# Optimization experiments

Measured on AMD Instinct MI355X. Metric: run time of the kernel, lower is better.

Reference implementation:

```python
import jax, jax.numpy as jnp
import numpy as np

N_HEADS = 16


def build_bd3lm_mask(n, block_size, dtype):
    """BD3LM mask for concatenated [xt | x0] input of length 2n.
    0 = attend, finfo.min = masked. Shape (2n, 2n)."""
    idx = jnp.arange(2 * n)
    q_idx = idx[:, None]
    kv_idx = idx[None, :]
    x0_q = q_idx >= n
    x0_kv = kv_idx >= n
    block_q = jnp.where(x0_q, (q_idx - n) // block_size, q_idx // block_size)
    block_kv = jnp.where(x0_kv, (kv_idx - n) // block_size, kv_idx // block_size)
    block_diagonal = (block_q == block_kv) & (x0_q == x0_kv)
    offset_block_causal = (block_q > block_kv) & x0_kv & (~x0_q)
    block_causal = (block_q >= block_kv) & x0_kv & x0_q
    can_attend = block_diagonal | offset_block_causal | block_causal
    neg = jnp.finfo(dtype).min
    return jnp.where(can_attend, jnp.array(0, dtype), jnp.array(neg, dtype))


def setup_inputs() -> dict:
    key = jax.random.key(0)
    ks = jax.random.split(key, 5)
    B, T, D = 4, 2048, 1024  # T = 2*L, L = 1024
    s = 1.0 / np.sqrt(D)
    return {
        "x": jax.random.normal(ks[0], (B, T, D), jnp.float32),
        "Wq": jax.random.normal(ks[1], (D, D), jnp.float32) * s,
        "bq": jnp.zeros((D,), jnp.float32),
        "Wk": jax.random.normal(ks[2], (D, D), jnp.float32) * s,
        "bk": jnp.zeros((D,), jnp.float32),
        "Wv": jax.random.normal(ks[3], (D, D), jnp.float32) * s,
        "bv": jnp.zeros((D,), jnp.float32),
        "Wo": jax.random.normal(ks[4], (D, D), jnp.float32) * s,
        "bo": jnp.zeros((D,), jnp.float32),
        "block_size": 4,
    }


def reference(x, Wq, bq, Wk, bk, Wv, bv, Wo, bo, block_size):
    B, T, D = x.shape
    H = N_HEADS
    hd = D // H
    n = T // 2  # length of each copy in [xt | x0]
    mask = build_bd3lm_mask(n, block_size, x.dtype)  # (T, T)

    def split_heads(t):  # (B, T, D) -> (B, H, T, hd)
        return t.reshape(B, T, H, hd).transpose(0, 2, 1, 3)

    q = split_heads(x @ Wq + bq) * (hd ** -0.5)
    k = split_heads(x @ Wk + bk)
    v = split_heads(x @ Wv + bv)
    scores = jnp.einsum("bhqd,bhkd->bhqk", q, k) + mask[None, None]
    attn = jax.nn.softmax(scores, axis=-1)
    ctx = jnp.einsum("bhqk,bhkd->bhqd", attn, v)
    ctx = ctx.transpose(0, 2, 1, 3).reshape(B, T, D)
    return ctx @ Wo + bo
```

## Files before the change

kernel.cpp:

```cpp
#include <hip/hip_runtime.h>
#include <hip/hip_bf16.h>
#include <stdint.h>

typedef __hip_bfloat16 bf16;
typedef short v8s __attribute__((ext_vector_type(8)));
typedef float v4f __attribute__((ext_vector_type(4)));

#define TT   2048
#define DD   1024
#define HH   16
#define HDIM 64
#define NN   1024
#define MASKV (-1e9f)
#define QSCALE 0.18033688011112042f

#if __has_builtin(__builtin_amdgcn_exp2f)
#define EXP2F(x) __builtin_amdgcn_exp2f(x)
#else
#define EXP2F(x) exp2f(x)
#endif

__device__ __forceinline__ v4f mfma16x16x32(v8s a, v8s b, v4f c) {
    return __builtin_amdgcn_mfma_f32_16x16x32_bf16(a, b, c, 0, 0, 0);
}

template<bool SW>
__device__ __forceinline__ v4f MM(v8s a, v8s b, v4f c) {
    if constexpr (SW)
        return __builtin_amdgcn_mfma_f32_16x16x32_bf16(b, a, c, 0, 0, 0);
    else
        return __builtin_amdgcn_mfma_f32_16x16x32_bf16(a, b, c, 0, 0, 0);
}

#define GLDS16(lds, g)                                                          \
    __builtin_amdgcn_global_load_lds(                                           \
        (const __attribute__((address_space(1))) void*)(g),                     \
        (__attribute__((address_space(3))) void*)(lds), 16, 0, 0)

__device__ __forceinline__ bf16 f2b(float f) { return __float2bfloat16(f); }

__global__ __launch_bounds__(256) void prep(
    const float* __restrict__ x,  bf16* __restrict__ xb,
    const float* __restrict__ w0, const float* __restrict__ w1,
    const float* __restrict__ w2, const float* __restrict__ w3,
    bf16* __restrict__ dst)
{
    __shared__ float tile[64][65];
    const int b = blockIdx.x, tid = threadIdx.x;

    if (b < 8192) {
        const size_t i = ((size_t)b * 256 + tid) * 4;
        const float4 f = *(const float4*)(x + i);
        union { bf16 bb[4]; uint64_t u; } cv;
        cv.bb[0] = f2b(f.x); cv.bb[1] = f2b(f.y);
        cv.bb[2] = f2b(f.z); cv.bb[3] = f2b(f.w);
        *(uint64_t*)(xb + i) = cv.u;
        return;
    }

    const int b2 = b - 8192;
    const int z  = b2 >> 8;
    const int rem = b2 & 255;
    const int c0 = (rem & 15) * 64, r0 = (rem >> 4) * 64;
    const float* src = (z == 0) ? w0 : (z == 1) ? w1 : (z == 2) ? w2 : w3;
    bf16* d = dst + (size_t)z * 1024 * 1024;
    const int tx = tid & 63, ty = tid >> 6;
#pragma unroll
    for (int j = 0; j < 16; j++) {
        int r = ty + j * 4;
        tile[r][tx] = src[(size_t)(r0 + r) * 1024 + c0 + tx];
    }
    __syncthreads();
#pragma unroll
    for (int j = 0; j < 16; j++) {
        int r = ty + j * 4;
        d[(size_t)(c0 + r) * 1024 + r0 + tx] = f2b(tile[tx][r]);
    }
}

template<bool SW>
__device__ __forceinline__ void gemm_core_256x128(
    const bf16* __restrict__ A, const bf16* __restrict__ BT,
    const int m0, const int n0, const int K,
    bf16* __restrict__ As, bf16* __restrict__ Bs,
    v4f (&acc)[8][2])
{
    const int tid  = threadIdx.x;
    const int lane = tid & 63, wv = tid >> 6;
    const int quad = lane >> 4, c = lane & 15;
    const int wm = wv >> 2, wn = wv & 3;
    const int c7 = c & 7;
    const int NT = K >> 6;

    const int rloc = wv * 8 + (lane >> 3);
    const int gsw  = ((lane & 7) ^ ((lane >> 3) & 7)) << 3;
    const bf16* aSrc = A  + (size_t)(m0 + rloc) * K + gsw;
    const bf16* bSrc = BT + (size_t)(n0 + rloc) * K + gsw;

#pragma unroll
    for (int i = 0; i < 8; i++)
#pragma unroll
        for (int j = 0; j < 2; j++) acc[i][j] = (v4f){0.f, 0.f, 0.f, 0.f};

    auto stageA = [&](bf16* dst, int j, int kt) {
        const int mo = ((j & 1) << 7) | ((j >> 1) << 6);
        GLDS16(dst + (j * 64 + wv * 8) * 64, aSrc + (size_t)mo * K + kt * 64);
    };
    auto stageB = [&](bf16* dst, int j, int kt) {
        GLDS16(dst + (j * 64 + wv * 8) * 64, bSrc + (size_t)(j << 6) * K + kt * 64);
    };

    stageB(Bs, 0, 0); stageB(Bs, 1, 0);
    stageA(As, 0, 0); stageA(As, 1, 0); stageA(As, 2, 0); stageA(As, 3, 0);
    asm volatile("s_waitcnt vmcnt(2)" ::: "memory");
    asm volatile("s_barrier" ::: "memory");

#pragma unroll 1
    for (int kt = 0; kt < NT; ++kt) {
        bf16* Ac = As + (kt & 1) * 16384;
        bf16* Bc = Bs + (kt & 1) * 8192;
        bf16* An = As + ((kt & 1) ^ 1) * 16384;
        bf16* Bn = Bs + ((kt & 1) ^ 1) * 8192;
        const int ktn = (kt + 1 < NT) ? kt + 1 : kt;

        v8s bfr[2][2];
#pragma unroll
        for (int nt = 0; nt < 2; nt++)
#pragma unroll
            for (int kh = 0; kh < 2; kh++)
                bfr[nt][kh] = *(const v8s*)(Bc + (wn * 32 + nt * 16 + c) * 64
                                            + (((kh * 4 + quad) ^ c7) << 3));
        v8s af[4][2];
#pragma unroll
        for (int mt = 0; mt < 4; mt++)
#pragma unroll
            for (int kh = 0; kh < 2; kh++)
                af[mt][kh] = *(const v8s*)(Ac + (wm * 64 + mt * 16 + c) * 64
                                           + (((kh * 4 + quad) ^ c7) << 3));
        stageB(Bn, 0, ktn); stageB(Bn, 1, ktn); stageA(An, 0, ktn);
        asm volatile("s_barrier" ::: "memory");
        __builtin_amdgcn_s_setprio(1);
#pragma unroll
        for (int mt = 0; mt < 4; mt++)
#pragma unroll
            for (int nt = 0; nt < 2; nt++) {
                acc[mt][nt] = MM<SW>(af[mt][0], bfr[nt][0], acc[mt][nt]);
                acc[mt][nt] = MM<SW>(af[mt][1], bfr[nt][1], acc[mt][nt]);
            }
        __builtin_amdgcn_s_setprio(0);
        asm volatile("s_waitcnt vmcnt(3)" ::: "memory");
        asm volatile("s_barrier" ::: "memory");

#pragma unroll
        for (int mt = 0; mt < 4; mt++)
#pragma unroll
            for (int kh = 0; kh < 2; kh++)
                af[mt][kh] = *(const v8s*)(Ac + (128 + wm * 64 + mt * 16 + c) * 64
                                           + (((kh * 4 + quad) ^ c7) << 3));
        stageA(An, 1, ktn); stageA(An, 2, ktn); stageA(An, 3, ktn);
        asm volatile("s_barrier" ::: "memory");
        __builtin_amdgcn_s_setprio(1);
#pragma unroll
        for (int mt = 0; mt < 4; mt++)
#pragma unroll
            for (int nt = 0; nt < 2; nt++) {
                acc[4 + mt][nt] = MM<SW>(af[mt][0], bfr[nt][0], acc[4 + mt][nt]);
                acc[4 + mt][nt] = MM<SW>(af[mt][1], bfr[nt][1], acc[4 + mt][nt]);
            }
        __builtin_amdgcn_s_setprio(0);
        asm volatile("s_waitcnt vmcnt(2)" ::: "memory");
        asm volatile("s_barrier" ::: "memory");
    }
    asm volatile("s_waitcnt vmcnt(0)" ::: "memory");
}

__global__ __launch_bounds__(512, 2) void gemm_qkv(
    const bf16* __restrict__ A, const bf16* __restrict__ BT,
    const float* __restrict__ bq, const float* __restrict__ bk,
    const float* __restrict__ bv,
    bf16* __restrict__ qo, bf16* __restrict__ ko, bf16* __restrict__ vt)
{
    __shared__ __align__(16) bf16 As[2 * 256 * 64];
    __shared__ __align__(16) bf16 Bs[2 * 128 * 64];
    const int id  = blockIdx.x;
    const int fid = (id & 7) * 96 + (id >> 3);
    const int by  = fid / 24, bx = fid - by * 24;
    const int m0  = by * 256, n0 = bx * 128;
    const int type = n0 >> 10;

    v4f acc[8][2];
    if (type == 2) gemm_core_256x128<true >(A, BT, m0, n0, 1024, As, Bs, acc);
    else           gemm_core_256x128<false>(A, BT, m0, n0, 1024, As, Bs, acc);

    const int tid  = threadIdx.x;
    const int lane = tid & 63, wv = tid >> 6;
    const int quad = lane >> 4, c = lane & 15;
    const int wm = wv >> 2, wn = wv & 3;
    const int nbase = n0 & 1023;

    if (type < 2) {
        bf16* o = (type == 0) ? qo : ko;
        const float* bp = (type == 0) ? bq : bk;
        const float scale = (type == 0) ? QSCALE : 1.0f;
#pragma unroll
        for (int mt = 0; mt < 8; mt++)
#pragma unroll
            for (int nt = 0; nt < 2; nt++) {
                const int within = nbase + wn * 32 + nt * 16 + c;
                const int h = within >> 6, d = within & 63;
                const float bias = bp[within];
#pragma unroll
                for (int r = 0; r < 4; r++) {
                    const int row = m0 + wm * 128 + mt * 16 + quad * 4 + r;
                    const int b_ = row >> 11, t = row & 2047;
                    const int bh = b_ * HH + h;
                    o[((size_t)bh * TT + t) * HDIM + d] =
                        f2b((acc[mt][nt][r] + bias) * scale);
                }
            }
    } else {
        const int b_    = m0 >> 11;
        const int m0loc = m0 & 2047;
#pragma unroll
        for (int mt = 0; mt < 8; mt++) {
            const int t = m0loc + wm * 128 + mt * 16 + c;
#pragma unroll
            for (int nt = 0; nt < 2; nt++)
#pragma unroll
                for (int r = 0; r < 4; r++) {
                    const int within = nbase + wn * 32 + nt * 16 + quad * 4 + r;
                    const int h = within >> 6, d = within & 63;
                    const int bh = b_ * HH + h;
                    vt[((size_t)bh * HDIM + d) * TT + t] =
                        f2b(acc[mt][nt][r] + bv[within]);
                }
        }
    }
}

__global__ __launch_bounds__(512, 2) void gemm_out(
    const bf16* __restrict__ A, const bf16* __restrict__ BT,
    const float* __restrict__ bo, float* __restrict__ out)
{
    __shared__ __align__(16) bf16 As[2 * 256 * 64];
    __shared__ __align__(16) bf16 Bs[2 * 128 * 64];
    const int id  = blockIdx.x;
    const int fid = (id & 7) * 32 + (id >> 3);
    const int by  = fid >> 3, bx = fid & 7;
    const int m0  = by * 256, n0 = bx * 128;

    v4f acc[8][2];
    gemm_core_256x128<false>(A, BT, m0, n0, 1024, As, Bs, acc);

    const int tid  = threadIdx.x;
    const int lane = tid & 63, wv = tid >> 6;
    const int quad = lane >> 4, c = lane & 15;
    const int wm = wv >> 2, wn = wv & 3;

#pragma unroll
    for (int mt = 0; mt < 8; mt++)
#pragma unroll
        for (int nt = 0; nt < 2; nt++) {
            const int col = n0 + wn * 32 + nt * 16 + c;
            const float bias = bo[col];
#pragma unroll
            for (int r = 0; r < 4; r++) {
                const int row = m0 + wm * 128 + mt * 16 + quad * 4 + r;
                out[(size_t)row * 1024 + col] = acc[mt][nt][r] + bias;
            }
        }
}

__global__ __launch_bounds__(512, 4) void attn(
    const bf16* __restrict__ Q, const bf16* __restrict__ Kb,
    const bf16* __restrict__ VT, bf16* __restrict__ ctx,
    const int* __restrict__ bsp)
{
    __shared__ __align__(16) bf16 Kt[2][32 * 64];
    __shared__ __align__(16) bf16 Vt[2][64 * 32];
    __shared__ __align__(16) bf16 plds[8][2][16 * 32];

    const int bs = bsp[0];
    const float inv  = 1.0f / (float)bs;
    const float hinv = 0.5f * inv;
    const int tid = threadIdx.x, lane = tid & 63, wv = tid >> 6;
    const int quad = lane >> 4, c = lane & 15;
    const int bh = blockIdx.x & 63;
    const int j  = blockIdx.x >> 6;
    const bool xt = j < 4;
    const int g  = xt ? (j ^ 3) : (j - 4);
    const int q0g = (xt ? 0 : NN) + g * 256;

    const bf16* qp = Q  + (size_t)bh * TT * HDIM;
    const bf16* kp = Kb + (size_t)bh * TT * HDIM;
    const bf16* vp = VT + (size_t)bh * HDIM * TT;

    int d_lo = 0, nd = 0, nf = 0, b_lo = 0, nb = 0;
    if (xt) {
        d_lo = (bs * (q0g / bs)) & ~31;
        const int d_hi = min((bs * ((q0g + 255) / bs) + bs + 31) & ~31, NN);
        nd = (d_hi - d_lo) >> 5;
        const int f = bs * (q0g / bs);
        nf = f >> 5;
        b_lo = NN + (nf << 5);
        const int b_hi = NN + min((bs * ((q0g + 255) / bs) + 31) & ~31, NN);
        nb = (b_hi > b_lo) ? (b_hi - b_lo) >> 5 : 0;
    } else {
        const int q0l = q0g - NN;
        const int f = min(bs * (q0l / bs) + bs, NN);
        nf = f >> 5;
        b_lo = NN + (nf << 5);
        const int b_hi = NN + min((bs * ((q0l + 255) / bs) + bs + 31) & ~31, NN);
        nb = (b_hi > b_lo) ? (b_hi - b_lo) >> 5 : 0;
    }
    const int nc = nd + nf + nb;

    float bqv[2][4];
#pragma unroll
    for (int t = 0; t < 2; t++)
#pragma unroll
        for (int r = 0; r < 4; r++) {
            const int qrow = q0g + wv * 32 + t * 16 + quad * 4 + r;
            const int qloc = xt ? qrow : qrow - NN;
            bqv[t][r] = floorf(fmaf((float)qloc, inv, hinv));
        }

    v8s aq[2][2];
#pragma unroll
    for (int t = 0; t < 2; t++) {
        const int rowb = q0g + wv * 32 + t * 16;
        aq[t][0] = *(const v8s*)(qp + (size_t)(rowb + c) * HDIM + quad * 8);
        aq[t][1] = *(const v8s*)(qp + (size_t)(rowb + c) * HDIM + 32 + quad * 8);
    }

    v4f O[2][4];
#pragma unroll
    for (int t = 0; t < 2; t++)
#pragma unroll
        for (int dt = 0; dt < 4; dt++) O[t][dt] = (v4f){0.f, 0.f, 0.f, 0.f};
    float lr[2][4] = {{0.f,0.f,0.f,0.f},{0.f,0.f,0.f,0.f}};

    const int w4 = wv & 3;
    const int klrow = lane >> 3;
    const bf16* kSrc0 = kp + (size_t)(w4 * 8 + klrow) * HDIM
                        + (((lane & 7) ^ klrow) << 3);
    const int vlrow = lane >> 2;
    const bf16* vSrc0 = vp + (size_t)(w4 * 16 + vlrow) * TT
                        + (((lane & 3) ^ (vlrow & 3)) << 3);

    auto kb_of = [&](int i, int& kb, int& type) {
        if (i < nd)           { kb = d_lo + (i << 5);             type = 1; }
        else if (i < nd + nf) { kb = NN + ((i - nd) << 5);        type = 0; }
        else                  { kb = b_lo + ((i - nd - nf) << 5); type = xt ? 2 : 3; }
    };
    auto stage = [&](int i) {
        int kb, ty; kb_of(i, kb, ty);
        const int sel = i & 1;
        if (wv < 4) GLDS16(&Kt[sel][w4 * 512], kSrc0 + (size_t)kb * HDIM);
        else        GLDS16(&Vt[sel][w4 * 512], vSrc0 + kb);
    };

    stage(0);
    asm volatile("s_waitcnt vmcnt(0)" ::: "memory");
    asm volatile("s_barrier" ::: "memory");

    const int xk = c & 7, xv = c & 3;
    const int pquad = quad << 3;
#pragma unroll 1
    for (int i = 0; i < nc; i++) {
        int kb, type; kb_of(i, kb, type);
        const int sel = i & 1;
        const bf16* Kl = Kt[sel];
        const bf16* Vl = Vt[sel];

        const v8s k0a = *(const v8s*)(Kl + c * 64        + ((quad       ^ xk) << 3));
        const v8s k0b = *(const v8s*)(Kl + c * 64        + (((quad ^ 4) ^ xk) << 3));
        const v8s k1a = *(const v8s*)(Kl + (16 + c) * 64 + ((quad       ^ xk) << 3));
        const v8s k1b = *(const v8s*)(Kl + (16 + c) * 64 + (((quad ^ 4) ^ xk) << 3));
        v8s vf[4];
#pragma unroll
        for (int dt = 0; dt < 4; dt++)
            vf[dt] = *(const v8s*)(Vl + (dt * 16 + c) * 32 + ((quad ^ xv) << 3));

        if (i + 1 < nc) stage(i + 1);

        float bkA = 0.f, bkB = 0.f;
        if (type) {
            const int off = (type == 1) ? 0 : NN;
            bkA = floorf(fmaf((float)(kb + c - off),      inv, hinv));
            bkB = floorf(fmaf((float)(kb + 16 + c - off), inv, hinv));
        }

#pragma unroll
        for (int t = 0; t < 2; t++) {
            v4f Sa = (v4f){0.f, 0.f, 0.f, 0.f};
            v4f Sb = (v4f){0.f, 0.f, 0.f, 0.f};
            Sa = mfma16x16x32(aq[t][0], k0a, Sa);
            Sa = mfma16x16x32(aq[t][1], k0b, Sa);
            Sb = mfma16x16x32(aq[t][0], k1a, Sb);
            Sb = mfma16x16x32(aq[t][1], k1b, Sb);
            bf16* pw = &plds[wv][t][(quad * 4) * 32];
#pragma unroll
            for (int r = 0; r < 4; r++) {
                float sa = Sa[r], sb = Sb[r];
                if (type == 1) {
                    if (bkA != bqv[t][r]) sa = MASKV;
                    if (bkB != bqv[t][r]) sb = MASKV;
                } else if (type == 2) {
                    if (!(bkA < bqv[t][r])) sa = MASKV;
                    if (!(bkB < bqv[t][r])) sb = MASKV;
                } else if (type == 3) {
                    if (!(bkA <= bqv[t][r])) sa = MASKV;
                    if (!(bkB <= bqv[t][r])) sb = MASKV;
                }
                const float pa = EXP2F(sa);
                const float pb = EXP2F(sb);
                lr[t][r] += pa + pb;
                pw[r * 32 + (c ^ pquad)]        = f2b(pa);
                pw[r * 32 + ((c + 16) ^ pquad)] = f2b(pb);
            }
        }
        asm volatile("s_waitcnt lgkmcnt(0)" ::: "memory");
#pragma unroll
        for (int t = 0; t < 2; t++) {
            const v8s pf = *(const v8s*)(&plds[wv][t][c * 32 +
                                        ((quad ^ ((c >> 2) & 3)) << 3)]);
#pragma unroll
            for (int dt = 0; dt < 4; dt++)
                O[t][dt] = mfma16x16x32(pf, vf[dt], O[t][dt]);
        }

        asm volatile("s_waitcnt vmcnt(0)" ::: "memory");
        asm volatile("s_barrier" ::: "memory");
    }

    const int b_ = bh >> 4, h = bh & 15;
#pragma unroll
    for (int t = 0; t < 2; t++)
#pragma unroll
        for (int r = 0; r < 4; r++) {
            float s = lr[t][r];
#pragma unroll
            for (int off = 1; off < 16; off <<= 1) s += __shfl_xor(s, off);
            const float invl = 1.0f / fmaxf(s, 1e-30f);
            const int trow = q0g + wv * 32 + t * 16 + quad * 4 + r;
#pragma unroll
            for (int dt = 0; dt < 4; dt++)
                ctx[((size_t)(b_ * TT + trow)) * DD + h * 64 + dt * 16 + c] =
                    f2b(O[t][dt][r] * invl);
        }
}

extern "C" void kernel_launch(void* const* d_in, const int* in_sizes, int n_in,
                              void* d_out, int out_size, void* d_ws, size_t ws_size,
                              hipStream_t stream)
{
    const float* x  = (const float*)d_in[0];
    const float* Wq = (const float*)d_in[1];
    const float* bq = (const float*)d_in[2];
    const float* Wk = (const float*)d_in[3];
    const float* bk = (const float*)d_in[4];
    const float* Wv = (const float*)d_in[5];
    const float* bv = (const float*)d_in[6];
    const float* Wo = (const float*)d_in[7];
    const float* bo = (const float*)d_in[8];
    const int*  bsp = (const int*)d_in[9];
    float* out = (float*)d_out;

    bf16* ws    = (bf16*)d_ws;
    bf16* xb    = ws;
    bf16* wqkvT = xb + 8388608;
    bf16* woT   = wqkvT + 3 * 1024 * 1024;
    bf16* qbuf  = woT + 1024 * 1024;
    bf16* kbuf  = qbuf + 8388608;
    bf16* vt    = kbuf + 8388608;
    bf16* ctx   = xb;

    prep<<<9216, 256, 0, stream>>>(x, xb, Wq, Wk, Wv, Wo, wqkvT);
    gemm_qkv<<<768, 512, 0, stream>>>(xb, wqkvT, bq, bk, bv, qbuf, kbuf, vt);
    attn<<<512, 512, 0, stream>>>(qbuf, kbuf, vt, ctx, bsp);
    gemm_out<<<256, 512, 0, stream>>>(ctx, woT, bo, out);
}
```

Baseline: 240.4 us.

## Use 256x256 tiles with 8-phase pipelined core for QKV GEMM

Replaces the 256x128 QKV projection GEMM with a 256x256 tile kernel. The new core splits each K-step into quarter-tile phases that interleave LDS fragment loads, global-to-LDS staging of the next K slice, and MFMA bursts. The goal is to raise arithmetic intensity per loaded byte and halve the grid to 384 blocks. It doubles the accumulator registers and B-side LDS, which may lower occupancy. It also leaves 384 blocks against 256 CUs, an uneven wave count.

```diff
diff --git a/kernel.cpp b/kernel.cpp
--- a/kernel.cpp
+++ b/kernel.cpp
@@ -36,6 +36,10 @@
     __builtin_amdgcn_global_load_lds(                                           \
         (const __attribute__((address_space(1))) void*)(g),                     \
         (__attribute__((address_space(3))) void*)(lds), 16, 0, 0)
+
+#define BARRIER()  asm volatile("s_barrier" ::: "memory")
+#define LGKM0()    asm volatile("s_waitcnt lgkmcnt(0)" ::: "memory")
+#define VMCNT(n)   asm volatile("s_waitcnt vmcnt(" #n ")" ::: "memory")
 
 __device__ __forceinline__ bf16 f2b(float f) { return __float2bfloat16(f); }
 
@@ -75,6 +79,277 @@
     for (int j = 0; j < 16; j++) {
         int r = ty + j * 4;
         d[(size_t)(c0 + r) * 1024 + r0 + tx] = f2b(tile[tx][r]);
+    }
+}
+
+template<bool SW>
+__device__ __forceinline__ void gemm_core_256sq(
+    const bf16* __restrict__ A, const bf16* __restrict__ BT,
+    const int m0, const int n0,
+    bf16* __restrict__ As, bf16* __restrict__ Bs,
+    v4f (&acc)[8][4])
+{
+    const int K = 1024;
+    const int tid  = threadIdx.x;
+    const int lane = tid & 63, wv = tid >> 6;
+    const int quad = lane >> 4, c = lane & 15;
+    const int wm = wv >> 2, wn = wv & 3;
+    const int c7 = c & 7;
+
+    const int r8 = lane >> 3;
+    const int gsw = ((lane & 7) ^ r8) << 3;
+    const bf16* aS = A  + (size_t)(m0 + wv * 8 + r8) * K + gsw;
+    const bf16* bS = BT + (size_t)(n0 + wv * 8 + r8) * K + gsw;
+
+    auto stA = [&](int slot, int q, int kt) {
+        GLDS16(As + slot * 16384 + (q * 64 + wv * 8) * 64,
+               aS + (size_t)(q * 64) * K + kt * 64);
+    };
+    auto stB = [&](int slot, int q, int kt) {
+        GLDS16(Bs + slot * 16384 + (q * 64 + wv * 8) * 64,
+               bS + (size_t)(q * 64) * K + kt * 64);
+    };
+
+#pragma unroll
+    for (int i = 0; i < 8; i++)
+#pragma unroll
+        for (int j = 0; j < 4; j++) acc[i][j] = (v4f){0.f, 0.f, 0.f, 0.f};
+
+    stA(0, 0, 0); stA(0, 1, 0); stA(0, 2, 0); stA(0, 3, 0);
+    stB(0, 0, 0); stB(0, 1, 0); stB(0, 2, 0); stB(0, 3, 0);
+    stA(1, 0, 1); stA(1, 1, 1);
+    VMCNT(2);
+    BARRIER();
+
+    v8s afr[4][2], bfr[2][2];
+
+    auto ldA = [&](const bf16* base, int mt, int kh) {
+        const int row = wm * 128 + mt * 16 + c;
+        return *(const v8s*)(base + row * 64 + (((kh * 4 + quad) ^ c7) << 3));
+    };
+    auto ldB = [&](const bf16* base, int nt, int kh) {
+        const int row = wn * 64 + nt * 16 + c;
+        return *(const v8s*)(base + row * 64 + (((kh * 4 + quad) ^ c7) << 3));
+    };
+
+#pragma unroll 1
+    for (int it = 0; it < 8; ++it) {
+        const int kt1 = 2 * it + 1;
+        const int kt2 = (2 * it + 2 < 16) ? 2 * it + 2 : 15;
+        const int kt3 = (2 * it + 3 < 16) ? 2 * it + 3 : 15;
+        const bf16* Ac0 = As;           const bf16* Bc0 = Bs;
+        const bf16* Ac1 = As + 16384;   const bf16* Bc1 = Bs + 16384;
+
+#pragma unroll
+        for (int mt = 0; mt < 4; mt++)
+#pragma unroll
+            for (int kh = 0; kh < 2; kh++) afr[mt][kh] = ldA(Ac0, mt, kh);
+#pragma unroll
+        for (int nt = 0; nt < 2; nt++)
+#pragma unroll
+            for (int kh = 0; kh < 2; kh++) bfr[nt][kh] = ldB(Bc0, nt, kh);
+        stA(1, 2, kt1); stA(1, 3, kt1);
+        BARRIER(); LGKM0();
+        __builtin_amdgcn_s_setprio(1);
+#pragma unroll
+        for (int mt = 0; mt < 4; mt++)
+#pragma unroll
+            for (int nt = 0; nt < 2; nt++) {
+                acc[mt][nt] = MM<SW>(afr[mt][0], bfr[nt][0], acc[mt][nt]);
+                acc[mt][nt] = MM<SW>(afr[mt][1], bfr[nt][1], acc[mt][nt]);
+            }
+        __builtin_amdgcn_s_setprio(0);
+        BARRIER();
+
+#pragma unroll
+        for (int nt = 0; nt < 2; nt++)
+#pragma unroll
+            for (int kh = 0; kh < 2; kh++) bfr[nt][kh] = ldB(Bc0, 2 + nt, kh);
+        stB(1, 0, kt1); stB(1, 1, kt1);
+        BARRIER(); LGKM0();
+        __builtin_amdgcn_s_setprio(1);
+#pragma unroll
+        for (int mt = 0; mt < 4; mt++)
+#pragma unroll
+            for (int nt = 0; nt < 2; nt++) {
+                acc[mt][2 + nt] = MM<SW>(afr[mt][0], bfr[nt][0], acc[mt][2 + nt]);
+                acc[mt][2 + nt] = MM<SW>(afr[mt][1], bfr[nt][1], acc[mt][2 + nt]);
+            }
+        __builtin_amdgcn_s_setprio(0);
+        BARRIER();
+
+#pragma unroll
+        for (int mt = 0; mt < 4; mt++)
+#pragma unroll
+            for (int kh = 0; kh < 2; kh++) afr[mt][kh] = ldA(Ac0, 4 + mt, kh);
+        stB(1, 2, kt1); stB(1, 3, kt1);
+        BARRIER(); LGKM0();
+        __builtin_amdgcn_s_setprio(1);
+#pragma unroll
+        for (int mt = 0; mt < 4; mt++)
+#pragma unroll
+            for (int nt = 0; nt < 2; nt++) {
+                acc[4 + mt][2 + nt] = MM<SW>(afr[mt][0], bfr[nt][0], acc[4 + mt][2 + nt]);
+                acc[4 + mt][2 + nt] = MM<SW>(afr[mt][1], bfr[nt][1], acc[4 + mt][2 + nt]);
+            }
+        __builtin_amdgcn_s_setprio(0);
+        BARRIER();
+
+#pragma unroll
+        for (int nt = 0; nt < 2; nt++)
+#pragma unroll
+            for (int kh = 0; kh < 2; kh++) bfr[nt][kh] = ldB(Bc0, nt, kh);
+        stA(0, 0, kt2); stA(0, 1, kt2);
+        BARRIER(); LGKM0();
+        __builtin_amdgcn_s_setprio(1);
+#pragma unroll
+        for (int mt = 0; mt < 4; mt++)
+#pragma unroll
+            for (int nt = 0; nt < 2; nt++) {
+                acc[4 + mt][nt] = MM<SW>(afr[mt][0], bfr[nt][0], acc[4 + mt][nt]);
+                acc[4 + mt][nt] = MM<SW>(afr[mt][1], bfr[nt][1], acc[4 + mt][nt]);
+            }
+        __builtin_amdgcn_s_setprio(0);
+        VMCNT(2);
+        BARRIER();
+
+#pragma unroll
+        for (int mt = 0; mt < 4; mt++)
+#pragma unroll
+            for (int kh = 0; kh < 2; kh++) afr[mt][kh] = ldA(Ac1, mt, kh);
+#pragma unroll
+        for (int nt = 0; nt < 2; nt++)
+#pragma unroll
+            for (int kh = 0; kh < 2; kh++) bfr[nt][kh] = ldB(Bc1, nt, kh);
+        stA(0, 2, kt2); stA(0, 3, kt2);
+        BARRIER(); LGKM0();
+        __builtin_amdgcn_s_setprio(1);
+#pragma unroll
+        for (int mt = 0; mt < 4; mt++)
+#pragma unroll
+            for (int nt = 0; nt < 2; nt++) {
+                acc[mt][nt] = MM<SW>(afr[mt][0], bfr[nt][0], acc[mt][nt]);
+                acc[mt][nt] = MM<SW>(afr[mt][1], bfr[nt][1], acc[mt][nt]);
+            }
+        __builtin_amdgcn_s_setprio(0);
+        BARRIER();
+
+#pragma unroll
+        for (int nt = 0; nt < 2; nt++)
+#pragma unroll
+            for (int kh = 0; kh < 2; kh++) bfr[nt][kh] = ldB(Bc1, 2 + nt, kh);
+        stB(0, 0, kt2); stB(0, 1, kt2);
+        BARRIER(); LGKM0();
+        __builtin_amdgcn_s_setprio(1);
+#pragma unroll
+        for (int mt = 0; mt < 4; mt++)
+#pragma unroll
+            for (int nt = 0; nt < 2; nt++) {
+                acc[mt][2 + nt] = MM<SW>(afr[mt][0], bfr[nt][0], acc[mt][2 + nt]);
+                acc[mt][2 + nt] = MM<SW>(afr[mt][1], bfr[nt][1], acc[mt][2 + nt]);
+            }
+        __builtin_amdgcn_s_setprio(0);
+        BARRIER();
+
+#pragma unroll
+        for (int mt = 0; mt < 4; mt++)
+#pragma unroll
+            for (int kh = 0; kh < 2; kh++) afr[mt][kh] = ldA(Ac1, 4 + mt, kh);
+        stB(0, 2, kt2); stB(0, 3, kt2);
+        BARRIER(); LGKM0();
+        __builtin_amdgcn_s_setprio(1);
+#pragma unroll
+        for (int mt = 0; mt < 4; mt++)
+#pragma unroll
+            for (int nt = 0; nt < 2; nt++) {
+                acc[4 + mt][2 + nt] = MM<SW>(afr[mt][0], bfr[nt][0], acc[4 + mt][2 + nt]);
+                acc[4 + mt][2 + nt] = MM<SW>(afr[mt][1], bfr[nt][1], acc[4 + mt][2 + nt]);
+            }
+        __builtin_amdgcn_s_setprio(0);
+        BARRIER();
+
+#pragma unroll
+        for (int nt = 0; nt < 2; nt++)
+#pragma unroll
+            for (int kh = 0; kh < 2; kh++) bfr[nt][kh] = ldB(Bc1, nt, kh);
+        stA(1, 0, kt3); stA(1, 1, kt3);
+        BARRIER(); LGKM0();
+        __builtin_amdgcn_s_setprio(1);
+#pragma unroll
+        for (int mt = 0; mt < 4; mt++)
+#pragma unroll
+            for (int nt = 0; nt < 2; nt++) {
+                acc[4 + mt][nt] = MM<SW>(afr[mt][0], bfr[nt][0], acc[4 + mt][nt]);
+                acc[4 + mt][nt] = MM<SW>(afr[mt][1], bfr[nt][1], acc[4 + mt][nt]);
+            }
+        __builtin_amdgcn_s_setprio(0);
+        VMCNT(2);
+        BARRIER();
+    }
+    asm volatile("s_waitcnt vmcnt(0)" ::: "memory");
+}
+
+__global__ __launch_bounds__(512, 2) void gemm_qkv(
+    const bf16* __restrict__ A, const bf16* __restrict__ BT,
+    const float* __restrict__ bq, const float* __restrict__ bk,
+    const float* __restrict__ bv,
+    bf16* __restrict__ qo, bf16* __restrict__ ko, bf16* __restrict__ vt)
+{
+    __shared__ __align__(16) bf16 As[2 * 256 * 64];
+    __shared__ __align__(16) bf16 Bs[2 * 256 * 64];
+    const int id  = blockIdx.x;
+    const int fid = (id & 7) * 48 + (id >> 3);
+    const int by  = fid / 12, bx = fid - by * 12;
+    const int m0  = by * 256, n0 = bx * 256;
+    const int type = n0 >> 10;
+
+    v4f acc[8][4];
+    if (type == 2) gemm_core_256sq<true >(A, BT, m0, n0, As, Bs, acc);
+    else           gemm_core_256sq<false>(A, BT, m0, n0, As, Bs, acc);
+
+    const int tid  = threadIdx.x;
+    const int lane = tid & 63, wv = tid >> 6;
+    const int quad = lane >> 4, c = lane & 15;
+    const int wm = wv >> 2, wn = wv & 3;
+    const int nbase = n0 & 1023;
+
+    if (type < 2) {
+        bf16* o = (type == 0) ? qo : ko;
+        const float* bp = (type == 0) ? bq : bk;
+        const float scale = (type == 0) ? QSCALE : 1.0f;
+#pragma unroll
+        for (int mt = 0; mt < 8; mt++)
+#pragma unroll
+            for (int nt = 0; nt < 4; nt++) {
+                const int within = nbase + wn * 64 + nt * 16 + c;
+                const int h = within >> 6, d = within & 63;
+                const float bias = bp[within];
+#pragma unroll
+                for (int r = 0; r < 4; r++) {
+                    const int row = m0 + wm * 128 + mt * 16 + quad * 4 + r;
+                    const int b_ = row >> 11, t = row & 2047;
+                    const int bh = b_ * HH + h;
+                    o[((size_t)bh * TT + t) * HDIM + d] =
+                        f2b((acc[mt][nt][r] + bias) * scale);
+                }
+            }
+    } else {
+        const int b_    = m0 >> 11;
+        const int m0loc = m0 & 2047;
+#pragma unroll
+        for (int mt = 0; mt < 8; mt++) {
+            const int t = m0loc + wm * 128 + mt * 16 + c;
+#pragma unroll
+            for (int nt = 0; nt < 4; nt++)
+#pragma unroll
+                for (int r = 0; r < 4; r++) {
+                    const int within = nbase + wn * 64 + nt * 16 + quad * 4 + r;
+                    const int h = within >> 6, d = within & 63;
+                    const int bh = b_ * HH + h;
+                    vt[((size_t)bh * HDIM + d) * TT + t] =
+                        f2b(acc[mt][nt][r] + bv[within]);
+                }
+        }
     }
 }
 
@@ -112,8 +387,8 @@
 
     stageB(Bs, 0, 0); stageB(Bs, 1, 0);
     stageA(As, 0, 0); stageA(As, 1, 0); stageA(As, 2, 0); stageA(As, 3, 0);
-    asm volatile("s_waitcnt vmcnt(2)" ::: "memory");
-    asm volatile("s_barrier" ::: "memory");
+    VMCNT(2);
+    BARRIER();
 
 #pragma unroll 1
     for (int kt = 0; kt < NT; ++kt) {
@@ -138,7 +413,7 @@
                 af[mt][kh] = *(const v8s*)(Ac + (wm * 64 + mt * 16 + c) * 64
                                            + (((kh * 4 + quad) ^ c7) << 3));
         stageB(Bn, 0, ktn); stageB(Bn, 1, ktn); stageA(An, 0, ktn);
-        asm volatile("s_barrier" ::: "memory");
+        BARRIER();
         __builtin_amdgcn_s_setprio(1);
 #pragma unroll
         for (int mt = 0; mt < 4; mt++)
@@ -148,8 +423,8 @@
                 acc[mt][nt] = MM<SW>(af[mt][1], bfr[nt][1], acc[mt][nt]);
             }
         __builtin_amdgcn_s_setprio(0);
-        asm volatile("s_waitcnt vmcnt(3)" ::: "memory");
-        asm volatile("s_barrier" ::: "memory");
+        VMCNT(3);
+        BARRIER();
 
 #pragma unroll
         for (int mt = 0; mt < 4; mt++)
@@ -158,7 +433,7 @@
                 af[mt][kh] = *(const v8s*)(Ac + (128 + wm * 64 + mt * 16 + c) * 64
                                            + (((kh * 4 + quad) ^ c7) << 3));
         stageA(An, 1, ktn); stageA(An, 2, ktn); stageA(An, 3, ktn);
-        asm volatile("s_barrier" ::: "memory");
+        BARRIER();
         __builtin_amdgcn_s_setprio(1);
 #pragma unroll
         for (int mt = 0; mt < 4; mt++)
@@ -168,74 +443,10 @@
                 acc[4 + mt][nt] = MM<SW>(af[mt][1], bfr[nt][1], acc[4 + mt][nt]);
             }
         __builtin_amdgcn_s_setprio(0);
-        asm volatile("s_waitcnt vmcnt(2)" ::: "memory");
-        asm volatile("s_barrier" ::: "memory");
+        VMCNT(2);
+        BARRIER();
     }
     asm volatile("s_waitcnt vmcnt(0)" ::: "memory");
-}
-
-__global__ __launch_bounds__(512, 2) void gemm_qkv(
-    const bf16* __restrict__ A, const bf16* __restrict__ BT,
-    const float* __restrict__ bq, const float* __restrict__ bk,
-    const float* __restrict__ bv,
-    bf16* __restrict__ qo, bf16* __restrict__ ko, bf16* __restrict__ vt)
-{
-    __shared__ __align__(16) bf16 As[2 * 256 * 64];
-    __shared__ __align__(16) bf16 Bs[2 * 128 * 64];
-    const int id  = blockIdx.x;
-    const int fid = (id & 7) * 96 + (id >> 3);
-    const int by  = fid / 24, bx = fid - by * 24;
-    const int m0  = by * 256, n0 = bx * 128;
-    const int type = n0 >> 10;
-
-    v4f acc[8][2];
-    if (type == 2) gemm_core_256x128<true >(A, BT, m0, n0, 1024, As, Bs, acc);
-    else           gemm_core_256x128<false>(A, BT, m0, n0, 1024, As, Bs, acc);
-
-    const int tid  = threadIdx.x;
-    const int lane = tid & 63, wv = tid >> 6;
-    const int quad = lane >> 4, c = lane & 15;
-    const int wm = wv >> 2, wn = wv & 3;
-    const int nbase = n0 & 1023;
-
-    if (type < 2) {
-        bf16* o = (type == 0) ? qo : ko;
-        const float* bp = (type == 0) ? bq : bk;
-        const float scale = (type == 0) ? QSCALE : 1.0f;
-#pragma unroll
-        for (int mt = 0; mt < 8; mt++)
-#pragma unroll
-            for (int nt = 0; nt < 2; nt++) {
-                const int within = nbase + wn * 32 + nt * 16 + c;
-                const int h = within >> 6, d = within & 63;
-                const float bias = bp[within];
-#pragma unroll
-                for (int r = 0; r < 4; r++) {
-                    const int row = m0 + wm * 128 + mt * 16 + quad * 4 + r;
-                    const int b_ = row >> 11, t = row & 2047;
-                    const int bh = b_ * HH + h;
-                    o[((size_t)bh * TT + t) * HDIM + d] =
-                        f2b((acc[mt][nt][r] + bias) * scale);
-                }
-            }
-    } else {
-        const int b_    = m0 >> 11;
-        const int m0loc = m0 & 2047;
-#pragma unroll
-        for (int mt = 0; mt < 8; mt++) {
-            const int t = m0loc + wm * 128 + mt * 16 + c;
-#pragma unroll
-            for (int nt = 0; nt < 2; nt++)
-#pragma unroll
-                for (int r = 0; r < 4; r++) {
-                    const int within = nbase + wn * 32 + nt * 16 + quad * 4 + r;
-                    const int h = within >> 6, d = within & 63;
-                    const int bh = b_ * HH + h;
-                    vt[((size_t)bh * HDIM + d) * TT + t] =
-                        f2b(acc[mt][nt][r] + bv[within]);
-                }
-        }
-    }
 }
 
 __global__ __launch_bounds__(512, 2) void gemm_out(
@@ -362,7 +573,7 @@
 
     stage(0);
     asm volatile("s_waitcnt vmcnt(0)" ::: "memory");
-    asm volatile("s_barrier" ::: "memory");
+    BARRIER();
 
     const int xk = c & 7, xv = c & 3;
     const int pquad = quad << 3;
@@ -431,7 +642,7 @@
         }
 
         asm volatile("s_waitcnt vmcnt(0)" ::: "memory");
-        asm volatile("s_barrier" ::: "memory");
+        BARRIER();
     }
 
     const int b_ = bh >> 4, h = bh & 15;
@@ -477,7 +688,7 @@
     bf16* ctx   = xb;
 
     prep<<<9216, 256, 0, stream>>>(x, xb, Wq, Wk, Wv, Wo, wqkvT);
-    gemm_qkv<<<768, 512, 0, stream>>>(xb, wqkvT, bq, bk, bv, qbuf, kbuf, vt);
+    gemm_qkv<<<384, 512, 0, stream>>>(xb, wqkvT, bq, bk, bv, qbuf, kbuf, vt);
     attn<<<512, 512, 0, stream>>>(qbuf, kbuf, vt, ctx, bsp);
     gemm_out<<<256, 512, 0, stream>>>(ctx, woT, bo, out);
 }
```

Result: slower. 256.1 us (+6.6%).
